# Optimization experiments

Hardware: AMD Instinct MI355X
Metric: run time of the kernel (lower is better)

Reference implementation:

```python
import jax, jax.numpy as jnp
import numpy as np

N = 200000
IN_F = 512
OUT_F = 256
NEG_INF = -9e15


def setup_inputs() -> dict:
    key = jax.random.key(0)
    k1, k2, k3, k4 = jax.random.split(key, 4)
    inp = jax.random.normal(k1, (N, IN_F), dtype=jnp.float32)
    adj = jax.random.randint(k2, (N, OUT_F), 0, 2, dtype=jnp.int32)
    # xavier_uniform with gain=1.414
    g = 1.414
    bW = g * np.sqrt(6.0 / (IN_F + OUT_F))
    W = jax.random.uniform(k3, (IN_F, OUT_F), jnp.float32, -bW, bW)
    ba = g * np.sqrt(6.0 / (2 * OUT_F + 1))
    a = jax.random.uniform(k4, (2 * OUT_F, 1), jnp.float32, -ba, ba)
    return {"input": inp, "adj": adj, "W": W, "a": a}


def reference(input, adj, W, a):
    h = input @ W                      # [N, M]
    M = h.shape[1]
    # a_input[n,m,:] = concat(h[n], h[n]) for every m, so
    # (a_input @ a)[n,m] = h[n] . (a[:M] + a[M:]) — constant over m.
    s = h @ (a[:M, 0] + a[M:, 0])      # [N]
    e = jax.nn.leaky_relu(s, negative_slope=0.2)[:, None]  # [N, 1]
    e = jnp.broadcast_to(e, (h.shape[0], M))               # [N, M]
    masked = jnp.where(adj > 0, e, NEG_INF)
    attention = jax.nn.softmax(masked, axis=1)             # rowwise softmax
    h_prime = attention * h                                # elementwise combine
    return jax.nn.elu(h_prime)
```

## Files before the change

kernel.cpp:

```cpp
#include <hip/hip_runtime.h>
#include <hip/hip_bf16.h>
#include <math.h>


#define R_TOTAL 200000
#define K_DIM   512
#define C_DIM   256
#define BM      64
#define BK      32
#define NCHUNK  (K_DIM / BK)
#define LSTR    40
#define CHUNK_BYTES (C_DIM * LSTR * 2)
#define WPACK_BYTES (NCHUNK * CHUNK_BYTES)

typedef __bf16 bf16x8 __attribute__((ext_vector_type(8)));
typedef __bf16 bf16x4 __attribute__((ext_vector_type(4)));
typedef float  f32x4  __attribute__((ext_vector_type(4)));

__global__ void prep_w(const float* __restrict__ W,
                       __bf16* __restrict__ whi, __bf16* __restrict__ wlo) {
  int idx = blockIdx.x * 256 + threadIdx.x;
  int k = idx >> 8, c = idx & 255;
  float w = W[idx];
  __bf16 h = (__bf16)w;
  __bf16 l = (__bf16)(w - (float)h);
  int off = ((k >> 5) * C_DIM + c) * LSTR + (k & 31);
  whi[off] = h;
  wlo[off] = l;
}

__device__ __forceinline__ void gload16(const void* g, void* l) {
  __builtin_amdgcn_global_load_lds(
      (const __attribute__((address_space(1))) unsigned*)g,
      (__attribute__((address_space(3))) unsigned*)l,
      16, 0, 0);
}

__global__ void __launch_bounds__(256)
gat_kernel(const float* __restrict__ X, const int* __restrict__ adj,
           const __bf16* __restrict__ whi, const __bf16* __restrict__ wlo,
           float* __restrict__ out) {
  __shared__ __bf16 Ah[BM * LSTR];
  __shared__ __bf16 Al[BM * LSTR];
  __shared__ __bf16 Bh[C_DIM * LSTR];
  __shared__ __bf16 Bl[C_DIM * LSTR];
  __shared__ float    invl[BM];
  __shared__ unsigned maskl[BM][8];

  const int tid  = threadIdx.x;
  const int lane = tid & 63;
  const int wv   = tid >> 6;
  const int wm   = wv >> 1;
  const int wn   = wv & 1;
  const int l15  = lane & 15;
  const int l4   = lane >> 4;
  const long r0  = (long)blockIdx.x * BM;

  {
    const int r = tid >> 2;
    const int q = tid & 3;
    const int4* ap = (const int4*)(adj + (r0 + r) * C_DIM + q * 64);
    unsigned w0 = 0, w1 = 0;
    int cnt = 0;
#pragma unroll
    for (int j = 0; j < 16; ++j) {
      int4 v = ap[j];
      unsigned b = 0;
      b |= (v.x > 0) ? 1u : 0u;
      b |= (v.y > 0) ? 2u : 0u;
      b |= (v.z > 0) ? 4u : 0u;
      b |= (v.w > 0) ? 8u : 0u;
      cnt += __popc(b);
      if (j < 8) w0 |= b << (j * 4);
      else       w1 |= b << ((j - 8) * 4);
    }
    cnt += __shfl_xor(cnt, 1);
    cnt += __shfl_xor(cnt, 2);
    if (cnt == 0) { w0 = 0xffffffffu; w1 = 0xffffffffu; }
    maskl[r][q * 2]     = w0;
    maskl[r][q * 2 + 1] = w1;
    if (q == 0) invl[r] = (cnt > 0) ? (1.0f / (float)cnt) : (1.0f / 256.0f);
  }

  f32x4 acc[2][8];
#pragma unroll
  for (int m = 0; m < 2; ++m)
#pragma unroll
    for (int n = 0; n < 8; ++n)
      acc[m][n] = f32x4{0.f, 0.f, 0.f, 0.f};

  const int sr = tid >> 3;
  const int sq = tid & 7;

  for (int ck = 0; ck < NCHUNK; ++ck) {
#pragma unroll
    for (int i = 0; i < 2; ++i) {
      int r = sr + i * 32;
      f32x4 v = *(const f32x4*)(X + (r0 + r) * K_DIM + ck * BK + sq * 4);
      bf16x4 hv, lv;
#pragma unroll
      for (int e = 0; e < 4; ++e) {
        float f = v[e];
        __bf16 hb = (__bf16)f;
        hv[e] = hb;
        lv[e] = (__bf16)(f - (float)hb);
      }
      *(bf16x4*)(&Ah[r * LSTR + sq * 4]) = hv;
      *(bf16x4*)(&Al[r * LSTR + sq * 4]) = lv;
    }
    {
      const char* srcH = (const char*)whi + ck * CHUNK_BYTES;
      const char* srcL = (const char*)wlo + ck * CHUNK_BYTES;
#pragma unroll
      for (int i = 0; i < 5; ++i) {
        int off = (wv * 5 + i) * 1024;
        gload16(srcH + off + lane * 16, (char*)Bh + off);
        gload16(srcL + off + lane * 16, (char*)Bl + off);
      }
    }
    __syncthreads();

    bf16x8 ahf[2], alf[2];
#pragma unroll
    for (int m = 0; m < 2; ++m) {
      int row = wm * 32 + m * 16 + l15;
      ahf[m] = *(const bf16x8*)(&Ah[row * LSTR + l4 * 8]);
      alf[m] = *(const bf16x8*)(&Al[row * LSTR + l4 * 8]);
    }
#pragma unroll
    for (int n = 0; n < 8; ++n) {
      int col = wn * 128 + n * 16 + l15;
      bf16x8 bh = *(const bf16x8*)(&Bh[col * LSTR + l4 * 8]);
      bf16x8 bl = *(const bf16x8*)(&Bl[col * LSTR + l4 * 8]);
#pragma unroll
      for (int m = 0; m < 2; ++m) {
        acc[m][n] = __builtin_amdgcn_mfma_f32_16x16x32_bf16(ahf[m], bh, acc[m][n], 0, 0, 0);
        acc[m][n] = __builtin_amdgcn_mfma_f32_16x16x32_bf16(ahf[m], bl, acc[m][n], 0, 0, 0);
        acc[m][n] = __builtin_amdgcn_mfma_f32_16x16x32_bf16(alf[m], bh, acc[m][n], 0, 0, 0);
      }
    }
    __syncthreads();
  }

#pragma unroll
  for (int m = 0; m < 2; ++m) {
#pragma unroll
    for (int n = 0; n < 8; ++n) {
      int col = wn * 128 + n * 16 + l15;
#pragma unroll
      for (int i = 0; i < 4; ++i) {
        int rl = wm * 32 + m * 16 + l4 * 4 + i;
        float inv = invl[rl];
        unsigned mw = maskl[rl][col >> 5];
        float h = acc[m][n][i];
        float o = 0.0f;
        if ((mw >> (col & 31)) & 1u) {
          float hp = h * inv;
          o = hp > 0.0f ? hp : expm1f(hp);
        }
        out[(r0 + rl) * C_DIM + col] = o;
      }
    }
  }
}

extern "C" void kernel_launch(void* const* d_in, const int* in_sizes, int n_in,
                              void* d_out, int out_size, void* d_ws, size_t ws_size,
                              hipStream_t stream) {
  const float* X   = (const float*)d_in[0];
  const int*   adj = (const int*)d_in[1];
  const float* W   = (const float*)d_in[2];
  __bf16* whi = (__bf16*)d_ws;
  __bf16* wlo = (__bf16*)((char*)d_ws + WPACK_BYTES);

  prep_w<<<512, 256, 0, stream>>>(W, whi, wlo);
  gat_kernel<<<R_TOTAL / BM, 256, 0, stream>>>(X, adj, whi, wlo, (float*)d_out);
}
```

Measured before the change: 846.7 us.

## Double-buffer LDS tiles, enlarge block to 128 rows, switch to 32x32 MFMA

Doubles the LDS buffers for the X and W chunks so the next chunk's global loads and bf16 split overlap the current chunk's MFMAs, with one barrier per chunk instead of two. The block grows to 128 rows and 512 threads, each wave owning a 32x128 output slice computed with 32x32x16 MFMAs. Tail rows are clamped and guarded because 200000 is not a multiple of 128. LDS use roughly doubles, which may lower occupancy, and the larger accumulator tiles raise register pressure.

```diff
diff --git a/kernel.cpp b/kernel.cpp
--- a/kernel.cpp
+++ b/kernel.cpp
@@ -3,19 +3,19 @@
 #include <math.h>
 
 
-#define R_TOTAL 200000
-#define K_DIM   512
-#define C_DIM   256
-#define BM      64
-#define BK      32
-#define NCHUNK  (K_DIM / BK)
-#define LSTR    40
+#define NROWS  200000
+#define K_DIM  512
+#define C_DIM  256
+#define BM     128
+#define BK     32
+#define NCHUNK 16
+#define LSTR   40
 #define CHUNK_BYTES (C_DIM * LSTR * 2)
 #define WPACK_BYTES (NCHUNK * CHUNK_BYTES)
 
 typedef __bf16 bf16x8 __attribute__((ext_vector_type(8)));
-typedef __bf16 bf16x4 __attribute__((ext_vector_type(4)));
 typedef float  f32x4  __attribute__((ext_vector_type(4)));
+typedef float  f32x16 __attribute__((ext_vector_type(16)));
 
 __global__ void prep_w(const float* __restrict__ W,
                        __bf16* __restrict__ whi, __bf16* __restrict__ wlo) {
@@ -32,18 +32,17 @@
 __device__ __forceinline__ void gload16(const void* g, void* l) {
   __builtin_amdgcn_global_load_lds(
       (const __attribute__((address_space(1))) unsigned*)g,
-      (__attribute__((address_space(3))) unsigned*)l,
-      16, 0, 0);
-}
-
-__global__ void __launch_bounds__(256)
+      (__attribute__((address_space(3))) unsigned*)l, 16, 0, 0);
+}
+
+__global__ void __launch_bounds__(512)
 gat_kernel(const float* __restrict__ X, const int* __restrict__ adj,
            const __bf16* __restrict__ whi, const __bf16* __restrict__ wlo,
            float* __restrict__ out) {
-  __shared__ __bf16 Ah[BM * LSTR];
-  __shared__ __bf16 Al[BM * LSTR];
-  __shared__ __bf16 Bh[C_DIM * LSTR];
-  __shared__ __bf16 Bl[C_DIM * LSTR];
+  __shared__ __bf16 Ah[2][BM * LSTR];
+  __shared__ __bf16 Al[2][BM * LSTR];
+  __shared__ __bf16 Bh[2][C_DIM * LSTR];
+  __shared__ __bf16 Bl[2][C_DIM * LSTR];
   __shared__ float    invl[BM];
   __shared__ unsigned maskl[BM][8];
 
@@ -52,27 +51,22 @@
   const int wv   = tid >> 6;
   const int wm   = wv >> 1;
   const int wn   = wv & 1;
-  const int l15  = lane & 15;
-  const int l4   = lane >> 4;
+  const int l31  = lane & 31;
+  const int hi   = lane >> 5;
   const long r0  = (long)blockIdx.x * BM;
 
   {
-    const int r = tid >> 2;
-    const int q = tid & 3;
-    const int4* ap = (const int4*)(adj + (r0 + r) * C_DIM + q * 64);
-    unsigned w0 = 0, w1 = 0;
-    int cnt = 0;
+    const int r = tid >> 2, q = tid & 3;
+    long rr = r0 + r; if (rr > NROWS - 1) rr = NROWS - 1;
+    const int4* ap = (const int4*)(adj + rr * C_DIM + q * 64);
+    unsigned w0 = 0, w1 = 0; int cnt = 0;
 #pragma unroll
     for (int j = 0; j < 16; ++j) {
       int4 v = ap[j];
-      unsigned b = 0;
-      b |= (v.x > 0) ? 1u : 0u;
-      b |= (v.y > 0) ? 2u : 0u;
-      b |= (v.z > 0) ? 4u : 0u;
-      b |= (v.w > 0) ? 8u : 0u;
+      unsigned b = (unsigned)((v.x > 0) | ((v.y > 0) << 1) |
+                              ((v.z > 0) << 2) | ((v.w > 0) << 3));
       cnt += __popc(b);
-      if (j < 8) w0 |= b << (j * 4);
-      else       w1 |= b << ((j - 8) * 4);
+      if (j < 8) w0 |= b << (j * 4); else w1 |= b << ((j - 8) * 4);
     }
     cnt += __shfl_xor(cnt, 1);
     cnt += __shfl_xor(cnt, 2);
@@ -82,83 +76,111 @@
     if (q == 0) invl[r] = (cnt > 0) ? (1.0f / (float)cnt) : (1.0f / 256.0f);
   }
 
-  f32x4 acc[2][8];
-#pragma unroll
-  for (int m = 0; m < 2; ++m)
-#pragma unroll
-    for (int n = 0; n < 8; ++n)
-      acc[m][n] = f32x4{0.f, 0.f, 0.f, 0.f};
-
-  const int sr = tid >> 3;
-  const int sq = tid & 7;
-
+  const int sr = tid >> 2;
+  const int sq = tid & 3;
+  long srow = r0 + sr; if (srow > NROWS - 1) srow = NROWS - 1;
+  const float* xbase = X + srow * K_DIM + sq * 8;
+  const int aoff = sr * LSTR + sq * 8;
+  const __bf16* bsrc = (wv < 4) ? whi : wlo;
+  const int bwq = wv & 3;
+
+  f32x16 acc[4];
+#pragma unroll
+  for (int n = 0; n < 4; ++n) acc[n] = (f32x16)(0.0f);
+
+  f32x4 xa, xb;
+  {
+    xa = *(const f32x4*)(xbase + 0);
+    xb = *(const f32x4*)(xbase + 4);
+    const char* s = (const char*)bsrc;
+    char* dh = (char*)((wv < 4) ? Bh[0] : Bl[0]);
+#pragma unroll
+    for (int i = 0; i < 5; ++i) {
+      int off = (bwq * 5 + i) * 1024;
+      gload16(s + off + lane * 16, dh + off);
+    }
+    bf16x8 hv, lv;
+#pragma unroll
+    for (int e = 0; e < 4; ++e) {
+      float f0 = xa[e], f1 = xb[e];
+      __bf16 h0 = (__bf16)f0, h1 = (__bf16)f1;
+      hv[e] = h0; hv[e + 4] = h1;
+      lv[e] = (__bf16)(f0 - (float)h0);
+      lv[e + 4] = (__bf16)(f1 - (float)h1);
+    }
+    *(bf16x8*)&Ah[0][aoff] = hv;
+    *(bf16x8*)&Al[0][aoff] = lv;
+  }
+  __syncthreads();
+
+  int cur = 0;
   for (int ck = 0; ck < NCHUNK; ++ck) {
-#pragma unroll
-    for (int i = 0; i < 2; ++i) {
-      int r = sr + i * 32;
-      f32x4 v = *(const f32x4*)(X + (r0 + r) * K_DIM + ck * BK + sq * 4);
-      bf16x4 hv, lv;
+    const bool pf = (ck + 1 < NCHUNK);
+    if (pf) {
+      xa = *(const f32x4*)(xbase + (ck + 1) * BK);
+      xb = *(const f32x4*)(xbase + (ck + 1) * BK + 4);
+      const char* s = (const char*)bsrc + (ck + 1) * CHUNK_BYTES;
+      char* dh = (char*)((wv < 4) ? Bh[cur ^ 1] : Bl[cur ^ 1]);
+#pragma unroll
+      for (int i = 0; i < 5; ++i) {
+        int off = (bwq * 5 + i) * 1024;
+        gload16(s + off + lane * 16, dh + off);
+      }
+    }
+#pragma unroll
+    for (int s2 = 0; s2 < 2; ++s2) {
+      const int ko = s2 * 16 + hi * 8;
+      bf16x8 ah = *(const bf16x8*)&Ah[cur][(wm * 32 + l31) * LSTR + ko];
+      bf16x8 al = *(const bf16x8*)&Al[cur][(wm * 32 + l31) * LSTR + ko];
+#pragma unroll
+      for (int n = 0; n < 4; ++n) {
+        const int coff = (wn * 128 + n * 32 + l31) * LSTR + ko;
+        bf16x8 bh = *(const bf16x8*)&Bh[cur][coff];
+        bf16x8 bl = *(const bf16x8*)&Bl[cur][coff];
+        acc[n] = __builtin_amdgcn_mfma_f32_32x32x16_bf16(ah, bh, acc[n], 0, 0, 0);
+        acc[n] = __builtin_amdgcn_mfma_f32_32x32x16_bf16(ah, bl, acc[n], 0, 0, 0);
+        acc[n] = __builtin_amdgcn_mfma_f32_32x32x16_bf16(al, bh, acc[n], 0, 0, 0);
+      }
+    }
+    if (pf) {
+      bf16x8 hv, lv;
 #pragma unroll
       for (int e = 0; e < 4; ++e) {
-        float f = v[e];
-        __bf16 hb = (__bf16)f;
-        hv[e] = hb;
-        lv[e] = (__bf16)(f - (float)hb);
-      }
-      *(bf16x4*)(&Ah[r * LSTR + sq * 4]) = hv;
-      *(bf16x4*)(&Al[r * LSTR + sq * 4]) = lv;
-    }
-    {
-      const char* srcH = (const char*)whi + ck * CHUNK_BYTES;
-      const char* srcL = (const char*)wlo + ck * CHUNK_BYTES;
-#pragma unroll
-      for (int i = 0; i < 5; ++i) {
-        int off = (wv * 5 + i) * 1024;
-        gload16(srcH + off + lane * 16, (char*)Bh + off);
-        gload16(srcL + off + lane * 16, (char*)Bl + off);
-      }
+        float f0 = xa[e], f1 = xb[e];
+        __bf16 h0 = (__bf16)f0, h1 = (__bf16)f1;
+        hv[e] = h0; hv[e + 4] = h1;
+        lv[e] = (__bf16)(f0 - (float)h0);
+        lv[e + 4] = (__bf16)(f1 - (float)h1);
+      }
+      *(bf16x8*)&Ah[cur ^ 1][aoff] = hv;
+      *(bf16x8*)&Al[cur ^ 1][aoff] = lv;
     }
     __syncthreads();
-
-    bf16x8 ahf[2], alf[2];
-#pragma unroll
-    for (int m = 0; m < 2; ++m) {
-      int row = wm * 32 + m * 16 + l15;
-      ahf[m] = *(const bf16x8*)(&Ah[row * LSTR + l4 * 8]);
-      alf[m] = *(const bf16x8*)(&Al[row * LSTR + l4 * 8]);
-    }
-#pragma unroll
-    for (int n = 0; n < 8; ++n) {
-      int col = wn * 128 + n * 16 + l15;
-      bf16x8 bh = *(const bf16x8*)(&Bh[col * LSTR + l4 * 8]);
-      bf16x8 bl = *(const bf16x8*)(&Bl[col * LSTR + l4 * 8]);
-#pragma unroll
-      for (int m = 0; m < 2; ++m) {
-        acc[m][n] = __builtin_amdgcn_mfma_f32_16x16x32_bf16(ahf[m], bh, acc[m][n], 0, 0, 0);
-        acc[m][n] = __builtin_amdgcn_mfma_f32_16x16x32_bf16(ahf[m], bl, acc[m][n], 0, 0, 0);
-        acc[m][n] = __builtin_amdgcn_mfma_f32_16x16x32_bf16(alf[m], bh, acc[m][n], 0, 0, 0);
-      }
-    }
-    __syncthreads();
-  }
-
-#pragma unroll
-  for (int m = 0; m < 2; ++m) {
-#pragma unroll
-    for (int n = 0; n < 8; ++n) {
-      int col = wn * 128 + n * 16 + l15;
-#pragma unroll
-      for (int i = 0; i < 4; ++i) {
-        int rl = wm * 32 + m * 16 + l4 * 4 + i;
-        float inv = invl[rl];
-        unsigned mw = maskl[rl][col >> 5];
-        float h = acc[m][n][i];
-        float o = 0.0f;
-        if ((mw >> (col & 31)) & 1u) {
-          float hp = h * inv;
-          o = hp > 0.0f ? hp : expm1f(hp);
+    cur ^= 1;
+  }
+
+#pragma unroll
+  for (int n = 0; n < 4; ++n) {
+    const int col = wn * 128 + n * 32 + l31;
+    const int mwi = col >> 5;
+#pragma unroll
+    for (int g = 0; g < 4; ++g) {
+#pragma unroll
+      for (int rb = 0; rb < 4; ++rb) {
+        const int reg = g * 4 + rb;
+        const int row = wm * 32 + rb + g * 8 + hi * 4;
+        const long rr = r0 + row;
+        if (rr < NROWS) {
+          float inv = invl[row];
+          unsigned mw = maskl[row][mwi];
+          float h = acc[n][reg];
+          float o = 0.0f;
+          if ((mw >> (col & 31)) & 1u) {
+            float hp = h * inv;
+            o = hp > 0.0f ? hp : expm1f(hp);
+          }
+          out[rr * C_DIM + col] = o;
         }
-        out[(r0 + rl) * C_DIM + col] = o;
       }
     }
   }
@@ -174,5 +196,6 @@
   __bf16* wlo = (__bf16*)((char*)d_ws + WPACK_BYTES);
 
   prep_w<<<512, 256, 0, stream>>>(W, whi, wlo);
-  gat_kernel<<<R_TOTAL / BM, 256, 0, stream>>>(X, adj, whi, wlo, (float*)d_out);
-}
+  const int nblk = (NROWS + BM - 1) / BM;
+  gat_kernel<<<nblk, 512, 0, stream>>>(X, adj, whi, wlo, (float*)d_out);
+}
```

Result: slower. 869.7 us (+2.7%).
